# Kernel tuning notes

Measured on AMD Instinct MI355X. Metric: run time of the kernel, lower is better.

Reference implementation:

```python
import jax, jax.numpy as jnp
import numpy as np

DIM = 1024
NH = 16
HD = DIM // NH  # 64
WS = 14         # window size
DFF = 4 * DIM
EPS = 1e-6


def layernorm(x, scale, bias):
    m = jnp.mean(x, axis=-1, keepdims=True)
    v = jnp.var(x, axis=-1, keepdims=True)
    return (x - m) * jax.lax.rsqrt(v + EPS) * scale + bias


def get_rel_pos(q_size, k_size, rel_pos):
    # table size (2*WS-1, HD) matches max_rel_dist, so no resize needed
    coords = (jnp.arange(q_size)[:, None] - jnp.arange(k_size)[None, :] + (k_size - 1)).astype(jnp.int32)
    return rel_pos[coords.reshape(-1)].reshape(q_size, k_size, -1)  # (q,k,HD)


def window_partition(x):
    b, h, w, c = x.shape
    pad_h = (WS - h % WS) % WS
    pad_w = (WS - w % WS) % WS
    # faithful to source: pad_w applied on axis 1, pad_h on axis 2
    x = jnp.pad(x, ((0, 0), (0, pad_w), (0, pad_h), (0, 0)))
    hp, wp = h + pad_h, w + pad_w
    x = x.reshape(b, hp // WS, WS, wp // WS, WS, c)
    windows = x.transpose(0, 1, 3, 2, 4, 5).reshape(-1, WS, WS, c)
    return windows, (hp, wp)


def window_unpartition(windows, pad_hw, hw):
    hp, wp = pad_hw
    h, w = hw
    b = windows.shape[0] // (hp * wp // WS // WS)
    x = windows.reshape(b, hp // WS, wp // WS, WS, WS, -1)
    x = x.transpose(0, 1, 3, 2, 4, 5).reshape(b, hp, wp, -1)
    return x[:, :h, :w, :]


def attention(x, qkv_kernel, qkv_bias, rel_pos_h, rel_pos_w, proj_kernel, proj_bias):
    b, h, w, _ = x.shape
    qkv = x @ qkv_kernel + qkv_bias                                  # (b,h,w,3*DIM)
    qkv = qkv.reshape(b, h * w, 3, NH, HD).transpose(2, 0, 3, 1, 4)
    qkv = qkv.reshape(3, b * NH, h * w, HD)
    q, k, v = qkv[0], qkv[1], qkv[2]
    attn = (q * HD ** -0.5) @ k.transpose(0, 2, 1)                   # (b*NH, hw, hw)
    rh = get_rel_pos(h, h, rel_pos_h)                                # (h,h,HD)
    rw = get_rel_pos(w, w, rel_pos_w)                                # (w,w,HD)
    r_q = q.reshape(-1, h, w, HD)
    rel_h = jnp.einsum('bhwc,hkc->bhwk', r_q, rh)
    rel_w = jnp.einsum('bhwc,wkc->bhwk', r_q, rw)
    attn = (attn.reshape(-1, h, w, h, w) + rel_h[:, :, :, :, None] + rel_w[:, :, :, None, :]).reshape(-1, h * w, h * w)
    attn = jax.nn.softmax(attn, axis=-1)
    out = (attn @ v).reshape(b, NH, h, w, HD).transpose(0, 2, 3, 1, 4).reshape(b, h, w, DIM)
    return out @ proj_kernel + proj_bias


def setup_inputs() -> dict:
    key = jax.random.key(0)
    ks = jax.random.split(key, 8)
    s = 0.02
    B, H, W = 4, 64, 64
    return {
        'x': jax.random.normal(ks[0], (B, H, W, DIM), jnp.float32),
        'norm1_scale': jnp.ones((DIM,), jnp.float32),
        'norm1_bias': jnp.zeros((DIM,), jnp.float32),
        'qkv_kernel': jax.random.normal(ks[1], (DIM, 3 * DIM), jnp.float32) * s,
        'qkv_bias': jnp.zeros((3 * DIM,), jnp.float32),
        'rel_pos_h': jax.random.normal(ks[2], (2 * WS - 1, HD), jnp.float32) * s,
        'rel_pos_w': jax.random.normal(ks[3], (2 * WS - 1, HD), jnp.float32) * s,
        'proj_kernel': jax.random.normal(ks[4], (DIM, DIM), jnp.float32) * s,
        'proj_bias': jnp.zeros((DIM,), jnp.float32),
        'norm2_scale': jnp.ones((DIM,), jnp.float32),
        'norm2_bias': jnp.zeros((DIM,), jnp.float32),
        'fc1_kernel': jax.random.normal(ks[5], (DIM, DFF), jnp.float32) * s,
        'fc1_bias': jnp.zeros((DFF,), jnp.float32),
        'fc2_kernel': jax.random.normal(ks[6], (DFF, DIM), jnp.float32) * s,
        'fc2_bias': jnp.zeros((DIM,), jnp.float32),
    }


def reference(x, norm1_scale, norm1_bias, qkv_kernel, qkv_bias, rel_pos_h, rel_pos_w,
              proj_kernel, proj_bias, norm2_scale, norm2_bias,
              fc1_kernel, fc1_bias, fc2_kernel, fc2_bias):
    shortcut = x
    h, w = x.shape[1], x.shape[2]
    y = layernorm(x, norm1_scale, norm1_bias)
    y, pad_hw = window_partition(y)
    y = attention(y, qkv_kernel, qkv_bias, rel_pos_h, rel_pos_w, proj_kernel, proj_bias)
    y = window_unpartition(y, pad_hw, (h, w))
    x = shortcut + y                           # drop_path=0, no layer scale
    z = layernorm(x, norm2_scale, norm2_bias)
    z = jax.nn.gelu(z @ fc1_kernel + fc1_bias, approximate=False)
    z = z @ fc2_kernel + fc2_bias
    return x + z
```

## Files before the change

### kernel.cpp

```cpp
#include <hip/hip_runtime.h>

typedef __attribute__((ext_vector_type(8))) short bf16x8;
typedef __attribute__((ext_vector_type(4))) float f32x4;
typedef __attribute__((ext_vector_type(16))) float f32x16;

__device__ __forceinline__ float b2f(ushort u) {
    union { unsigned int i; float f; } v; v.i = ((unsigned int)u) << 16; return v.f;
}
__device__ __forceinline__ ushort f2b(float f) {
    union { float f; unsigned int i; } v; v.f = f;
    unsigned int i = v.i;
    return (ushort)((i + 0x7FFFu + ((i >> 16) & 1u)) >> 16);
}
__device__ __forceinline__ void glds16(const ushort* g, ushort* l) {
    __builtin_amdgcn_global_load_lds((const __attribute__((address_space(1))) void*)g,
                                     (__attribute__((address_space(3))) void*)l, 16, 0, 0);
}
__device__ __forceinline__ void BARX() {
    asm volatile("" ::: "memory");
    __builtin_amdgcn_s_barrier();
    asm volatile("" ::: "memory");
}

__global__ __launch_bounds__(256) void ln_kernel(const float* __restrict__ x,
                                                 const float* __restrict__ sc,
                                                 const float* __restrict__ bi,
                                                 ushort* __restrict__ y) {
    __shared__ float red[8];
    long row = blockIdx.x;
    const float* xr = x + row * 1024;
    int t = threadIdx.x;
    float4 u = *(const float4*)(xr + t * 4);
    float s = u.x + u.y + u.z + u.w;
    float q = u.x * u.x + u.y * u.y + u.z * u.z + u.w * u.w;
    for (int off = 32; off > 0; off >>= 1) {
        s += __shfl_xor(s, off);
        q += __shfl_xor(q, off);
    }
    if ((t & 63) == 0) { red[t >> 6] = s; red[4 + (t >> 6)] = q; }
    __syncthreads();
    s = red[0] + red[1] + red[2] + red[3];
    q = red[4] + red[5] + red[6] + red[7];
    float mean = s * (1.0f / 1024.0f);
    float var = q * (1.0f / 1024.0f) - mean * mean;
    float rstd = rsqrtf(fmaxf(var, 0.0f) + 1e-6f);
    int c = t * 4;
    float o0 = (u.x - mean) * rstd * sc[c + 0] + bi[c + 0];
    float o1 = (u.y - mean) * rstd * sc[c + 1] + bi[c + 1];
    float o2 = (u.z - mean) * rstd * sc[c + 2] + bi[c + 2];
    float o3 = (u.w - mean) * rstd * sc[c + 3] + bi[c + 3];
    uint2 o;
    o.x = (unsigned int)f2b(o0) | ((unsigned int)f2b(o1) << 16);
    o.y = (unsigned int)f2b(o2) | ((unsigned int)f2b(o3) << 16);
    *(uint2*)(y + row * 1024 + c) = o;
}

__global__ __launch_bounds__(256) void ln_part_kernel(const float* __restrict__ x,
                                                      const float* __restrict__ sc,
                                                      const float* __restrict__ bi,
                                                      ushort* __restrict__ wy,
                                                      int win_base, int nvalid) {
    __shared__ float red[8];
    int wt = blockIdx.x;
    int lwin = wt / 196, rr = wt % 196;
    int t = threadIdx.x;
    int valid = 0;
    long xrow = 0;
    if (lwin < nvalid) {
        int gwin = win_base + lwin;
        int img = gwin / 25, wrem = gwin % 25;
        int gh = (wrem / 5) * 14 + rr / 14;
        int gw = (wrem % 5) * 14 + rr % 14;
        if (gh < 64 && gw < 64) {
            valid = 1;
            xrow = (long)img * 4096 + gh * 64 + gw;
        }
    }
    uint2 o; o.x = 0u; o.y = 0u;
    if (valid) {
        const float* xr = x + xrow * 1024;
        float4 u = *(const float4*)(xr + t * 4);
        float s = u.x + u.y + u.z + u.w;
        float q = u.x * u.x + u.y * u.y + u.z * u.z + u.w * u.w;
        for (int off = 32; off > 0; off >>= 1) {
            s += __shfl_xor(s, off);
            q += __shfl_xor(q, off);
        }
        if ((t & 63) == 0) { red[t >> 6] = s; red[4 + (t >> 6)] = q; }
        __syncthreads();
        s = red[0] + red[1] + red[2] + red[3];
        q = red[4] + red[5] + red[6] + red[7];
        float mean = s * (1.0f / 1024.0f);
        float var = q * (1.0f / 1024.0f) - mean * mean;
        float rstd = rsqrtf(fmaxf(var, 0.0f) + 1e-6f);
        int c = t * 4;
        float o0 = (u.x - mean) * rstd * sc[c + 0] + bi[c + 0];
        float o1 = (u.y - mean) * rstd * sc[c + 1] + bi[c + 1];
        float o2 = (u.z - mean) * rstd * sc[c + 2] + bi[c + 2];
        float o3 = (u.w - mean) * rstd * sc[c + 3] + bi[c + 3];
        o.x = (unsigned int)f2b(o0) | ((unsigned int)f2b(o1) << 16);
        o.y = (unsigned int)f2b(o2) | ((unsigned int)f2b(o3) << 16);
    }
    *(uint2*)(wy + (long)wt * 1024 + t * 4) = o;
}

__global__ void transpose_w(const float* __restrict__ in, ushort* __restrict__ out,
                            int K, int N) {
    __shared__ float tile[32][33];
    int n0 = blockIdx.x * 32, k0 = blockIdx.y * 32;
    int tx = threadIdx.x, ty = threadIdx.y;
    for (int i = 0; i < 32; i += 8)
        tile[ty + i][tx] = in[(long)(k0 + ty + i) * N + n0 + tx];
    __syncthreads();
    for (int i = 0; i < 32; i += 8)
        out[(long)(n0 + ty + i) * K + k0 + tx] = f2b(tile[tx][ty + i]);
}

template <int FLAGS, typename OT>
__global__ __launch_bounds__(256) void gemm_bt(const ushort* __restrict__ A,
                                               const ushort* __restrict__ Bt,
                                               const float* __restrict__ bias,
                                               const float* __restrict__ resid,
                                               OT* __restrict__ out,
                                               int M, int N, int K) {
    __shared__ __align__(16) ushort As[128 * 32];
    __shared__ __align__(16) ushort Bs[128 * 32];
    const int tid = threadIdx.x;
    const int lane = tid & 63, w = tid >> 6;
    const int wm = (w >> 1) * 64, wn = (w & 1) * 64;
    const int quad = lane >> 4, l16 = lane & 15;
    const int bm = blockIdx.x * 128, bn = blockIdx.y * 128;
    const int r = tid >> 2, kc = (tid & 3) * 8;
    f32x4 acc[4][4];
#pragma unroll
    for (int i = 0; i < 4; i++)
#pragma unroll
        for (int j = 0; j < 4; j++) acc[i][j] = (f32x4){0.f, 0.f, 0.f, 0.f};
    const ushort* Ag = A + (long)(bm + r) * K + kc;
    const ushort* Bg = Bt + (long)(bn + r) * K + kc;
    ushort* AsW = As + w * 512;
    ushort* BsW = Bs + w * 512;
    for (int k0 = 0; k0 < K; k0 += 32) {
        __syncthreads();
        glds16(Ag + k0, AsW);
        glds16(Ag + (long)64 * K + k0, AsW + 2048);
        glds16(Bg + k0, BsW);
        glds16(Bg + (long)64 * K + k0, BsW + 2048);
        __syncthreads();
        bf16x8 afr[4], bfr[4];
#pragma unroll
        for (int t = 0; t < 4; t++) {
            afr[t] = *(const bf16x8*)&As[(wm + t * 16 + l16) * 32 + quad * 8];
            bfr[t] = *(const bf16x8*)&Bs[(wn + t * 16 + l16) * 32 + quad * 8];
        }
#pragma unroll
        for (int tm = 0; tm < 4; tm++)
#pragma unroll
            for (int tn = 0; tn < 4; tn++)
                acc[tm][tn] = __builtin_amdgcn_mfma_f32_16x16x32_bf16(afr[tm], bfr[tn],
                                                                     acc[tm][tn], 0, 0, 0);
    }
#pragma unroll
    for (int tm = 0; tm < 4; tm++) {
#pragma unroll
        for (int j = 0; j < 4; j++) {
            int gm = bm + wm + tm * 16 + quad * 4 + j;
#pragma unroll
            for (int tn = 0; tn < 4; tn++) {
                int gn = bn + wn + tn * 16 + l16;
                float v = acc[tm][tn][j] + bias[gn];
                if (FLAGS & 1) v = 0.5f * v * (1.0f + erff(v * 0.70710678118654752f));
                if (FLAGS & 2) v += resid[(long)gm * N + gn];
                if (sizeof(OT) == 4) out[(long)gm * N + gn] = (OT)v;
                else out[(long)gm * N + gn] = (OT)f2b(v);
            }
        }
    }
}

#define DSR(dst, addr, imm) \
    asm volatile("ds_read_b128 %0, %1 offset:%2" : "=&v"(dst) : "v"(addr), "n"(imm));

#define MFMA32(mf, nf, a, b) \
    acc[mf][nf] = __builtin_amdgcn_mfma_f32_32x32x16_bf16(a, b, acc[mf][nf], 0, 0, 0);

#define TILE32(bb, ts, STG, VM) do {                                                     \
    bf16x8 b00, b10, a00, a10, a20, a30, b01, b11, a01, a11, a21, a31;                   \
    DSR(b00, b_k0, (bb) * 16384 + 0)                                                     \
    DSR(b10, b_k0, (bb) * 16384 + 2048)                                                  \
    DSR(a00, a_k0, (bb) * 16384 + 0)                                                     \
    DSR(a10, a_k0, (bb) * 16384 + 2048)                                                  \
    DSR(a20, a_k0, (bb) * 16384 + 4096)                                                  \
    DSR(a30, a_k0, (bb) * 16384 + 6144)                                                  \
    DSR(b01, b_k1, (bb) * 16384 + 0)                                                     \
    DSR(b11, b_k1, (bb) * 16384 + 2048)                                                  \
    DSR(a01, a_k1, (bb) * 16384 + 0)                                                     \
    DSR(a11, a_k1, (bb) * 16384 + 2048)                                                  \
    DSR(a21, a_k1, (bb) * 16384 + 4096)                                                  \
    DSR(a31, a_k1, (bb) * 16384 + 6144)                                                  \
    if (STG) {                                                                           \
        glds16(Ag + (long)(ts) * 32, &As[((bb) + 3) & 3][sdst]);                         \
        glds16(Ag2 + (long)(ts) * 32, &As[((bb) + 3) & 3][sdst + 4096]);                 \
        glds16(Bg + (long)(ts) * 32, &Bs[((bb) + 3) & 3][sdst]);                         \
        glds16(Bg2 + (long)(ts) * 32, &Bs[((bb) + 3) & 3][sdst + 4096]);                 \
    }                                                                                    \
    __builtin_amdgcn_sched_barrier(0);                                                   \
    asm volatile("s_waitcnt lgkmcnt(6)" ::: "memory");                                   \
    __builtin_amdgcn_sched_barrier(0);                                                   \
    __builtin_amdgcn_s_setprio(1);                                                       \
    MFMA32(0, 0, a00, b00) MFMA32(0, 1, a00, b10)                                        \
    MFMA32(1, 0, a10, b00) MFMA32(1, 1, a10, b10)                                        \
    MFMA32(2, 0, a20, b00) MFMA32(2, 1, a20, b10)                                        \
    MFMA32(3, 0, a30, b00) MFMA32(3, 1, a30, b10)                                        \
    __builtin_amdgcn_s_setprio(0);                                                       \
    asm volatile("s_waitcnt lgkmcnt(0)" ::: "memory");                                   \
    __builtin_amdgcn_sched_barrier(0);                                                   \
    __builtin_amdgcn_s_setprio(1);                                                       \
    MFMA32(0, 0, a01, b01) MFMA32(0, 1, a01, b11)                                        \
    MFMA32(1, 0, a11, b01) MFMA32(1, 1, a11, b11)                                        \
    MFMA32(2, 0, a21, b01) MFMA32(2, 1, a21, b11)                                        \
    MFMA32(3, 0, a31, b01) MFMA32(3, 1, a31, b11)                                        \
    __builtin_amdgcn_s_setprio(0);                                                       \
    __builtin_amdgcn_sched_barrier(0);                                                   \
    asm volatile("s_waitcnt " VM ::: "memory");                                          \
    BARX();                                                                              \
} while (0)

template <int FLAGS, typename OT>
__global__ __launch_bounds__(512, 2) void gemm256(const ushort* __restrict__ A,
                                                  const ushort* __restrict__ Bt,
                                                  const float* __restrict__ bias,
                                                  const float* __restrict__ resid,
                                                  OT* __restrict__ out,
                                                  int M, int N, int K, int nbn) {
    __shared__ __align__(64) ushort As[4][8192];
    __shared__ __align__(64) ushort Bs[4][8192];
    const int nwg = gridDim.x;
    const int orig = blockIdx.x;
    const int q8 = nwg >> 3, r8 = nwg & 7;
    const int xcd = orig & 7, sub = orig >> 3;
    const int wgid = (xcd < r8 ? xcd * (q8 + 1) : r8 * (q8 + 1) + (xcd - r8) * q8) + sub;
    const int bm = (wgid / nbn) * 256, bn = (wgid % nbn) * 256;

    const int tid = threadIdx.x;
    const int lane = tid & 63, w = tid >> 6;
    const int l31 = lane & 31, hi = lane >> 5;
    const int wm = (w >> 2) * 128, wn = (w & 3) * 64;

    const int r_st = w * 16 + (lane >> 2);
    const int c_st = (((lane & 3) ^ ((lane >> 2) & 3) ^ ((lane >> 4) & 1)) << 3);
    const ushort* Ag = A + (long)(bm + r_st) * K + c_st;
    const ushort* Ag2 = Ag + (long)128 * K;
    const ushort* Bg = Bt + (long)(bn + r_st) * K + c_st;
    const ushort* Bg2 = Bg + (long)128 * K;
    const int sdst = w * 512;

    const int swz = (lane & 3) ^ ((lane >> 2) & 1);
    const int s0 = swz & 1, s1 = swz >> 1;
    const int slot_k0 = (((0 ^ s1) << 1) | (hi ^ s0)) << 4;
    const int slot_k1 = (((1 ^ s1) << 1) | (hi ^ s0)) << 4;
    const unsigned As0 =
        (unsigned)(size_t)(__attribute__((address_space(3))) ushort*)&As[0][0];
    const unsigned Bs0 =
        (unsigned)(size_t)(__attribute__((address_space(3))) ushort*)&Bs[0][0];
    const unsigned a_k0 = As0 + (unsigned)((wm + l31) * 64 + slot_k0);
    const unsigned a_k1 = As0 + (unsigned)((wm + l31) * 64 + slot_k1);
    const unsigned b_k0 = Bs0 + (unsigned)((wn + l31) * 64 + slot_k0);
    const unsigned b_k1 = Bs0 + (unsigned)((wn + l31) * 64 + slot_k1);

    f32x16 acc[4][2];
#pragma unroll
    for (int i = 0; i < 4; i++)
#pragma unroll
        for (int j = 0; j < 2; j++)
#pragma unroll
            for (int e = 0; e < 16; e++) acc[i][j][e] = 0.f;

    glds16(Ag, &As[0][sdst]);       glds16(Ag2, &As[0][sdst + 4096]);
    glds16(Bg, &Bs[0][sdst]);       glds16(Bg2, &Bs[0][sdst + 4096]);
    glds16(Ag + 32, &As[1][sdst]);  glds16(Ag2 + 32, &As[1][sdst + 4096]);
    glds16(Bg + 32, &Bs[1][sdst]);  glds16(Bg2 + 32, &Bs[1][sdst + 4096]);
    glds16(Ag + 64, &As[2][sdst]);  glds16(Ag2 + 64, &As[2][sdst + 4096]);
    glds16(Bg + 64, &Bs[2][sdst]);  glds16(Bg2 + 64, &Bs[2][sdst + 4096]);
    __builtin_amdgcn_sched_barrier(0);
    asm volatile("s_waitcnt vmcnt(8)" ::: "memory");
    BARX();

    const int nt = K >> 5;
    for (int t = 0; t < nt - 4; t += 4) {
        TILE32(0, t + 3, 1, "vmcnt(8)");
        TILE32(1, t + 4, 1, "vmcnt(8)");
        TILE32(2, t + 5, 1, "vmcnt(8)");
        TILE32(3, t + 6, 1, "vmcnt(8)");
    }
    TILE32(0, nt - 1, 1, "vmcnt(8)");
    TILE32(1, 0, 0, "vmcnt(4)");
    TILE32(2, 0, 0, "vmcnt(0)");
    TILE32(3, 0, 0, "vmcnt(0)");

#pragma unroll
    for (int mf = 0; mf < 4; mf++) {
#pragma unroll
        for (int nf = 0; nf < 2; nf++) {
            const int gn = bn + wn + nf * 32 + l31;
#pragma unroll
            for (int q = 0; q < 4; q++) {
#pragma unroll
                for (int j = 0; j < 4; j++) {
                    const int gm = bm + wm + mf * 32 + q * 8 + j + 4 * hi;
                    const long ro = (long)gm * N;
                    float v = acc[mf][nf][q * 4 + j] + bias[gn];
                    if (FLAGS & 1) v = 0.5f * v * (1.0f + erff(v * 0.70710678118654752f));
                    if (FLAGS & 2) v += resid[ro + gn];
                    if (sizeof(OT) == 4) out[ro + gn] = (OT)v;
                    else out[ro + gn] = (OT)f2b(v);
                }
            }
        }
    }
}

__global__ __launch_bounds__(256) void attn_kernel(const ushort* __restrict__ qkv,
                                                   ushort* __restrict__ o_out,
                                                   const float* __restrict__ relH,
                                                   const float* __restrict__ relW,
                                                   int win0, long orow0) {
    __shared__ __align__(16) ushort Vt[64 * 200];
    __shared__ __align__(16) ushort Ps[64 * 104];
    __shared__ __align__(16) ushort sc[8 * 448];
    const int head = blockIdx.y;
    const long qbase = (long)blockIdx.x * 196 * 3072 + head * 64;
    const int gwin = win0 + blockIdx.x;
    const int img = gwin / 25, wrem = gwin % 25;
    const int whh = (wrem / 5) * 14, www = (wrem % 5) * 14;
    const int tid = threadIdx.x, lane = tid & 63, w = tid >> 6;
    const int quad = lane >> 4, l16 = lane & 15;

    for (int idx = tid; idx < 196 * 64; idx += 256) {
        int k = idx >> 6, d = idx & 63;
        Vt[d * 200 + k] = qkv[qbase + 2048 + (long)k * 3072 + d];
    }
    __syncthreads();

    bf16x8 bH[2][2], bW[2][2];
#pragma unroll
    for (int nt = 0; nt < 2; nt++) {
        int n = nt * 16 + l16;
#pragma unroll
        for (int kt = 0; kt < 2; kt++) {
            bf16x8 rh = (bf16x8){0, 0, 0, 0, 0, 0, 0, 0};
            bf16x8 rw = (bf16x8){0, 0, 0, 0, 0, 0, 0, 0};
            if (n < 27) {
                const float* ph = relH + n * 64 + kt * 32 + quad * 8;
                const float* pw = relW + n * 64 + kt * 32 + quad * 8;
#pragma unroll
                for (int e = 0; e < 8; e++) {
                    rh[e] = (short)f2b(ph[e]);
                    rw[e] = (short)f2b(pw[e]);
                }
            }
            bH[nt][kt] = rh;
            bW[nt][kt] = rw;
        }
    }

    for (int tr = w; tr < 13; tr += 4) {
        int qrow = tr * 16 + l16;
        if (qrow > 195) qrow = 195;
        bf16x8 qf0 = *(const bf16x8*)(qkv + qbase + (long)qrow * 3072 + quad * 8);
        bf16x8 qf1 = *(const bf16x8*)(qkv + qbase + (long)qrow * 3072 + 32 + quad * 8);

#pragma unroll
        for (int tab = 0; tab < 2; tab++) {
#pragma unroll
            for (int nt = 0; nt < 2; nt++) {
                f32x4 a = (f32x4){0.f, 0.f, 0.f, 0.f};
                a = __builtin_amdgcn_mfma_f32_16x16x32_bf16(qf0, tab ? bW[nt][0] : bH[nt][0],
                                                            a, 0, 0, 0);
                a = __builtin_amdgcn_mfma_f32_16x16x32_bf16(qf1, tab ? bW[nt][1] : bH[nt][1],
                                                            a, 0, 0, 0);
                int col = nt * 16 + l16;
                if (col < 27) {
#pragma unroll
                    for (int j = 0; j < 4; j++)
                        sc[(w * 2 + tab) * 448 + (quad * 4 + j) * 28 + col] = f2b(a[j]);
                }
            }
        }

        f32x4 sf[13];
#pragma unroll
        for (int tc = 0; tc < 13; tc++) {
            int krow = tc * 16 + l16;
            if (krow > 195) krow = 195;
            const ushort* kp = qkv + qbase + 1024 + (long)krow * 3072 + quad * 8;
            bf16x8 kf0 = *(const bf16x8*)kp;
            bf16x8 kf1 = *(const bf16x8*)(kp + 32);
            f32x4 s = (f32x4){0.f, 0.f, 0.f, 0.f};
            s = __builtin_amdgcn_mfma_f32_16x16x32_bf16(qf0, kf0, s, 0, 0, 0);
            s = __builtin_amdgcn_mfma_f32_16x16x32_bf16(qf1, kf1, s, 0, 0, 0);
            sf[tc] = s;
        }
#pragma unroll
        for (int tc = 0; tc < 13; tc++) {
            int c = tc * 16 + l16;
            if (c < 196) {
                int kh = c / 14, kw = c - kh * 14;
#pragma unroll
                for (int j = 0; j < 4; j++) {
                    int rr = tr * 16 + quad * 4 + j;
                    if (rr > 195) rr = 195;
                    float dh = b2f(sc[(w * 2 + 0) * 448 + (quad * 4 + j) * 28 +
                                      (rr / 14 - kh + 13)]);
                    float dw = b2f(sc[(w * 2 + 1) * 448 + (quad * 4 + j) * 28 +
                                      (rr % 14 - kw + 13)]);
                    sf[tc][j] = sf[tc][j] * 0.125f + dh + dw;
                }
            } else {
#pragma unroll
                for (int j = 0; j < 4; j++) sf[tc][j] = -30000.0f;
            }
        }
        f32x4 mx = sf[0];
#pragma unroll
        for (int tc = 1; tc < 13; tc++)
#pragma unroll
            for (int j = 0; j < 4; j++) mx[j] = fmaxf(mx[j], sf[tc][j]);
        for (int off = 1; off < 16; off <<= 1)
#pragma unroll
            for (int j = 0; j < 4; j++) mx[j] = fmaxf(mx[j], __shfl_xor(mx[j], off));
        f32x4 sum = (f32x4){0.f, 0.f, 0.f, 0.f};
#pragma unroll
        for (int tc = 0; tc < 13; tc++)
#pragma unroll
            for (int j = 0; j < 4; j++) {
                float p = __expf(sf[tc][j] - mx[j]);
                sf[tc][j] = p;
                sum[j] += p;
            }
        for (int off = 1; off < 16; off <<= 1)
#pragma unroll
            for (int j = 0; j < 4; j++) sum[j] += __shfl_xor(sum[j], off);
        f32x4 linv;
#pragma unroll
        for (int j = 0; j < 4; j++) linv[j] = 1.0f / sum[j];

        f32x4 oa[4];
#pragma unroll
        for (int tn = 0; tn < 4; tn++) oa[tn] = (f32x4){0.f, 0.f, 0.f, 0.f};
#pragma unroll
        for (int tc = 0; tc < 6; tc++) {
            int c = tc * 16 + l16;
#pragma unroll
            for (int j = 0; j < 4; j++)
                Ps[(w * 16 + quad * 4 + j) * 104 + c] = f2b(sf[tc][j]);
        }
#pragma unroll
        for (int ks = 0; ks < 3; ks++) {
            bf16x8 pf = *(const bf16x8*)&Ps[(w * 16 + l16) * 104 + ks * 32 + quad * 8];
#pragma unroll
            for (int tn = 0; tn < 4; tn++) {
                bf16x8 vf = *(const bf16x8*)&Vt[(tn * 16 + l16) * 200 + ks * 32 + quad * 8];
                oa[tn] = __builtin_amdgcn_mfma_f32_16x16x32_bf16(pf, vf, oa[tn], 0, 0, 0);
            }
        }
#pragma unroll
        for (int tc = 6; tc < 13; tc++) {
            int c = tc * 16 + l16;
            if (c < 196) {
#pragma unroll
                for (int j = 0; j < 4; j++)
                    Ps[(w * 16 + quad * 4 + j) * 104 + (c - 96)] = f2b(sf[tc][j]);
            }
        }
#pragma unroll
        for (int ks = 0; ks < 3; ks++) {
            bf16x8 pf = *(const bf16x8*)&Ps[(w * 16 + l16) * 104 + ks * 32 + quad * 8];
#pragma unroll
            for (int tn = 0; tn < 4; tn++) {
                bf16x8 vf = *(const bf16x8*)&Vt[(tn * 16 + l16) * 200 + 96 + ks * 32 + quad * 8];
                oa[tn] = __builtin_amdgcn_mfma_f32_16x16x32_bf16(pf, vf, oa[tn], 0, 0, 0);
            }
        }
        for (int kk = 192; kk < 196; kk++) {
            float pj[4];
#pragma unroll
            for (int j = 0; j < 4; j++)
                pj[j] = b2f(Ps[(w * 16 + quad * 4 + j) * 104 + 96 + (kk - 192)]);
#pragma unroll
            for (int tn = 0; tn < 4; tn++) {
                float vv = b2f(Vt[(tn * 16 + l16) * 200 + kk]);
#pragma unroll
                for (int j = 0; j < 4; j++) oa[tn][j] += pj[j] * vv;
            }
        }
#pragma unroll
        for (int j = 0; j < 4; j++) {
            int rr = tr * 16 + quad * 4 + j;
            if (rr < 196) {
                int gh = whh + rr / 14, gw = www + rr % 14;
                if (gh < 64 && gw < 64) {
                    long orow = (long)img * 4096 + gh * 64 + gw - orow0;
#pragma unroll
                    for (int tn = 0; tn < 4; tn++)
                        o_out[orow * 1024 + head * 64 + tn * 16 + l16] =
                            f2b(oa[tn][j] * linv[j]);
                }
            }
        }
    }
}

extern "C" void kernel_launch(void* const* d_in, const int* in_sizes, int n_in,
                              void* d_out, int out_size, void* d_ws, size_t ws_size,
                              hipStream_t stream) {
    const float* x = (const float*)d_in[0];
    const float* n1s = (const float*)d_in[1];
    const float* n1b = (const float*)d_in[2];
    const float* qkvW = (const float*)d_in[3];
    const float* qkvB = (const float*)d_in[4];
    const float* relH = (const float*)d_in[5];
    const float* relW = (const float*)d_in[6];
    const float* projW = (const float*)d_in[7];
    const float* projB = (const float*)d_in[8];
    const float* n2s = (const float*)d_in[9];
    const float* n2b = (const float*)d_in[10];
    const float* fc1W = (const float*)d_in[11];
    const float* fc1B = (const float*)d_in[12];
    const float* fc2W = (const float*)d_in[13];
    const float* fc2B = (const float*)d_in[14];
    float* OUT = (float*)d_out;
    char* ws = (char*)d_ws;

    if (ws_size >= 221000000ULL) {
        ushort* T0  = (ushort*)(ws);
        ushort* TP  = (ushort*)(ws + 6291456ULL);
        ushort* TF1 = (ushort*)(ws + 8388608ULL);
        ushort* TF2 = (ushort*)(ws + 16777216ULL);
        ushort* W0  = (ushort*)(ws + 25165824ULL);
        ushort* QKV = (ushort*)(ws + 65536000ULL);
        ushort* AO  = (ushort*)(ws + 186646528ULL);
        ushort* Z   = (ushort*)(ws + 25165824ULL);
        ushort* H   = (ushort*)(ws + 58720256ULL);

        transpose_w<<<dim3(96, 32), dim3(32, 8), 0, stream>>>(qkvW, T0, 1024, 3072);
        transpose_w<<<dim3(32, 32), dim3(32, 8), 0, stream>>>(projW, TP, 1024, 1024);
        transpose_w<<<dim3(128, 32), dim3(32, 8), 0, stream>>>(fc1W, TF1, 1024, 4096);
        transpose_w<<<dim3(32, 128), dim3(32, 8), 0, stream>>>(fc2W, TF2, 4096, 1024);
        ln_part_kernel<<<19712, 256, 0, stream>>>(x, n1s, n1b, W0, 0, 100);
        gemm256<0, ushort><<<924, 512, 0, stream>>>(W0, T0, qkvB, nullptr, QKV,
                                                    19712, 3072, 1024, 12);
        attn_kernel<<<dim3(100, 16), 256, 0, stream>>>(QKV, AO, relH, relW, 0, 0L);
        gemm256<2, float><<<256, 512, 0, stream>>>(AO, TP, projB, x, OUT,
                                                   16384, 1024, 1024, 4);
        ln_kernel<<<16384, 256, 0, stream>>>(OUT, n2s, n2b, Z);
        gemm256<1, ushort><<<1024, 512, 0, stream>>>(Z, TF1, fc1B, nullptr, H,
                                                     16384, 4096, 1024, 16);
        gemm256<2, float><<<256, 512, 0, stream>>>(H, TF2, fc2B, OUT, OUT,
                                                   16384, 1024, 4096, 4);
    } else if (ws_size >= 100000000ULL) {
        ushort* T0  = (ushort*)(ws);
        ushort* TP  = (ushort*)(ws + 6291456ULL);
        ushort* TF1 = (ushort*)(ws + 8388608ULL);
        ushort* TF2 = (ushort*)(ws + 16777216ULL);
        ushort* AO  = (ushort*)(ws + 25165824ULL);
        ushort* W0  = (ushort*)(ws + 58720256ULL);
        ushort* QKV = (ushort*)(ws + 68943872ULL);
        ushort* Z   = (ushort*)(ws + 25165824ULL);
        ushort* H   = (ushort*)(ws + 58720256ULL);

        transpose_w<<<dim3(96, 32), dim3(32, 8), 0, stream>>>(qkvW, T0, 1024, 3072);
        transpose_w<<<dim3(32, 32), dim3(32, 8), 0, stream>>>(projW, TP, 1024, 1024);
        transpose_w<<<dim3(128, 32), dim3(32, 8), 0, stream>>>(fc1W, TF1, 1024, 4096);
        transpose_w<<<dim3(32, 128), dim3(32, 8), 0, stream>>>(fc2W, TF2, 4096, 1024);
        for (int i = 0; i < 4; i++) {
            ln_part_kernel<<<4992, 256, 0, stream>>>(x, n1s, n1b, W0, i * 25, 25);
            gemm_bt<0, ushort><<<dim3(39, 24), 256, 0, stream>>>(W0, T0, qkvB, nullptr,
                                                                 QKV, 4992, 3072, 1024);
            attn_kernel<<<dim3(25, 16), 256, 0, stream>>>(QKV, AO, relH, relW, i * 25, 0L);
        }
        gemm_bt<2, float><<<dim3(128, 8), 256, 0, stream>>>(AO, TP, projB, x, OUT,
                                                            16384, 1024, 1024);
        for (int c = 0; c < 4; c++) {
            float* xc = OUT + (long)c * 4194304;
            ln_kernel<<<4096, 256, 0, stream>>>(xc, n2s, n2b, Z);
            gemm_bt<1, ushort><<<dim3(32, 32), 256, 0, stream>>>(Z, TF1, fc1B, nullptr, H,
                                                                 4096, 4096, 1024);
            gemm_bt<2, float><<<dim3(32, 8), 256, 0, stream>>>(H, TF2, fc2B, xc, xc,
                                                               4096, 1024, 4096);
        }
    } else {
        ushort* T0 = (ushort*)(ws);
        ushort* W0 = (ushort*)(ws + 6291456ULL);
        ushort* W1 = (ushort*)(ws + 16515072ULL);
        ushort* W2 = (ushort*)(ws + 22806528ULL);
        ushort* F1 = (ushort*)(ws);
        ushort* F2 = (ushort*)(ws + 8388608ULL);
        ushort* Z  = (ushort*)(ws + 16777216ULL);
        ushort* H  = (ushort*)(ws + 18874368ULL);

        transpose_w<<<dim3(96, 32), dim3(32, 8), 0, stream>>>(qkvW, T0, 1024, 3072);
        for (int i = 0; i < 4; i++) {
            const float* xi = x + (long)i * 4194304;
            ln_part_kernel<<<4992, 256, 0, stream>>>(x, n1s, n1b, W0, i * 25, 25);
            for (int g = 0; g < 5; g++) {
                gemm_bt<0, ushort><<<dim3(8, 24), 256, 0, stream>>>(
                    W0 + (long)g * 980 * 1024, T0, qkvB, nullptr, W1, 1024, 3072, 1024);
                attn_kernel<<<dim3(5, 16), 256, 0, stream>>>(W1, W2, relH, relW,
                                                             i * 25 + g * 5, (long)i * 4096);
            }
            transpose_w<<<dim3(32, 32), dim3(32, 8), 0, stream>>>(projW, W1, 1024, 1024);
            gemm_bt<2, float><<<dim3(32, 8), 256, 0, stream>>>(
                W2, W1, projB, xi, OUT + (long)i * 4194304, 4096, 1024, 1024);
        }
        transpose_w<<<dim3(128, 32), dim3(32, 8), 0, stream>>>(fc1W, F1, 1024, 4096);
        transpose_w<<<dim3(32, 128), dim3(32, 8), 0, stream>>>(fc2W, F2, 4096, 1024);
        for (int c = 0; c < 16; c++) {
            float* xc = OUT + (long)c * 1048576;
            ln_kernel<<<1024, 256, 0, stream>>>(xc, n2s, n2b, Z);
            gemm_bt<1, ushort><<<dim3(8, 32), 256, 0, stream>>>(Z, F1, fc1B, nullptr, H,
                                                                1024, 4096, 1024);
            gemm_bt<2, float><<<dim3(8, 8), 256, 0, stream>>>(H, F2, fc2B, xc, xc,
                                                              1024, 1024, 4096);
        }
    }
}
```

Measured before the change: 901.8 us.

## Software-pipeline LDS fragment reads across k-halves and tiles in gemm256

Restructures the GEMM main loop so the LDS reads for the next k-half (including the first half of the next buffer) are issued before the MFMAs of the current half run. This overlaps ds_read latency with matrix work, and global-to-LDS staging is issued at the start of each tile. It doubles the live fragment registers, reorders the vmcnt waits, and rewrites the loop tail by hand. Register pressure and the correctness of the wait counts around the barrier are the main risks.

```diff
diff --git a/kernel.cpp b/kernel.cpp
--- a/kernel.cpp
+++ b/kernel.cpp
@@ -184,45 +184,49 @@
 #define MFMA32(mf, nf, a, b) \
     acc[mf][nf] = __builtin_amdgcn_mfma_f32_32x32x16_bf16(a, b, acc[mf][nf], 0, 0, 0);
 
-#define TILE32(bb, ts, STG, VM) do {                                                     \
-    bf16x8 b00, b10, a00, a10, a20, a30, b01, b11, a01, a11, a21, a31;                   \
-    DSR(b00, b_k0, (bb) * 16384 + 0)                                                     \
-    DSR(b10, b_k0, (bb) * 16384 + 2048)                                                  \
-    DSR(a00, a_k0, (bb) * 16384 + 0)                                                     \
-    DSR(a10, a_k0, (bb) * 16384 + 2048)                                                  \
-    DSR(a20, a_k0, (bb) * 16384 + 4096)                                                  \
-    DSR(a30, a_k0, (bb) * 16384 + 6144)                                                  \
-    DSR(b01, b_k1, (bb) * 16384 + 0)                                                     \
-    DSR(b11, b_k1, (bb) * 16384 + 2048)                                                  \
-    DSR(a01, a_k1, (bb) * 16384 + 0)                                                     \
-    DSR(a11, a_k1, (bb) * 16384 + 2048)                                                  \
-    DSR(a21, a_k1, (bb) * 16384 + 4096)                                                  \
-    DSR(a31, a_k1, (bb) * 16384 + 6144)                                                  \
-    if (STG) {                                                                           \
-        glds16(Ag + (long)(ts) * 32, &As[((bb) + 3) & 3][sdst]);                         \
-        glds16(Ag2 + (long)(ts) * 32, &As[((bb) + 3) & 3][sdst + 4096]);                 \
-        glds16(Bg + (long)(ts) * 32, &Bs[((bb) + 3) & 3][sdst]);                         \
-        glds16(Bg2 + (long)(ts) * 32, &Bs[((bb) + 3) & 3][sdst + 4096]);                 \
-    }                                                                                    \
+#define RDK0(buf) \
+    DSR(y0, b_k0, (buf) * 16384 + 0)    DSR(y1, b_k0, (buf) * 16384 + 2048) \
+    DSR(x0, a_k0, (buf) * 16384 + 0)    DSR(x1, a_k0, (buf) * 16384 + 2048) \
+    DSR(x2, a_k0, (buf) * 16384 + 4096) DSR(x3, a_k0, (buf) * 16384 + 6144)
+
+#define RDK1(buf) \
+    DSR(Y0, b_k1, (buf) * 16384 + 0)    DSR(Y1, b_k1, (buf) * 16384 + 2048) \
+    DSR(X0, a_k1, (buf) * 16384 + 0)    DSR(X1, a_k1, (buf) * 16384 + 2048) \
+    DSR(X2, a_k1, (buf) * 16384 + 4096) DSR(X3, a_k1, (buf) * 16384 + 6144)
+
+#define MFK0 \
+    MFMA32(0, 0, x0, y0) MFMA32(0, 1, x0, y1) MFMA32(1, 0, x1, y0) MFMA32(1, 1, x1, y1) \
+    MFMA32(2, 0, x2, y0) MFMA32(2, 1, x2, y1) MFMA32(3, 0, x3, y0) MFMA32(3, 1, x3, y1)
+
+#define MFK1 \
+    MFMA32(0, 0, X0, Y0) MFMA32(0, 1, X0, Y1) MFMA32(1, 0, X1, Y0) MFMA32(1, 1, X1, Y1) \
+    MFMA32(2, 0, X2, Y0) MFMA32(2, 1, X2, Y1) MFMA32(3, 0, X3, Y0) MFMA32(3, 1, X3, Y1)
+
+#define LGW6 asm volatile("s_waitcnt lgkmcnt(6)" ::: "memory"); \
+    __builtin_amdgcn_sched_barrier(0);
+
+#define STAGE4(ts, dbuf) \
+    glds16(Ag + (long)(ts) * 32, &As[dbuf][sdst]); \
+    glds16(Ag2 + (long)(ts) * 32, &As[dbuf][sdst + 4096]); \
+    glds16(Bg + (long)(ts) * 32, &Bs[dbuf][sdst]); \
+    glds16(Bg2 + (long)(ts) * 32, &Bs[dbuf][sdst + 4096]);
+
+#define TILEF(bb, ts) do {                                                               \
+    STAGE4(ts + 3, ((bb) + 3) & 3)                                                       \
     __builtin_amdgcn_sched_barrier(0);                                                   \
-    asm volatile("s_waitcnt lgkmcnt(6)" ::: "memory");                                   \
-    __builtin_amdgcn_sched_barrier(0);                                                   \
+    asm volatile("s_waitcnt vmcnt(4)" ::: "memory");                                     \
+    RDK1(bb)                                                                             \
+    LGW6                                                                                 \
     __builtin_amdgcn_s_setprio(1);                                                       \
-    MFMA32(0, 0, a00, b00) MFMA32(0, 1, a00, b10)                                        \
-    MFMA32(1, 0, a10, b00) MFMA32(1, 1, a10, b10)                                        \
-    MFMA32(2, 0, a20, b00) MFMA32(2, 1, a20, b10)                                        \
-    MFMA32(3, 0, a30, b00) MFMA32(3, 1, a30, b10)                                        \
-    __builtin_amdgcn_s_setprio(0);                                                       \
-    asm volatile("s_waitcnt lgkmcnt(0)" ::: "memory");                                   \
-    __builtin_amdgcn_sched_barrier(0);                                                   \
-    __builtin_amdgcn_s_setprio(1);                                                       \
-    MFMA32(0, 0, a01, b01) MFMA32(0, 1, a01, b11)                                        \
-    MFMA32(1, 0, a11, b01) MFMA32(1, 1, a11, b11)                                        \
-    MFMA32(2, 0, a21, b01) MFMA32(2, 1, a21, b11)                                        \
-    MFMA32(3, 0, a31, b01) MFMA32(3, 1, a31, b11)                                        \
+    MFK0                                                                                 \
     __builtin_amdgcn_s_setprio(0);                                                       \
     __builtin_amdgcn_sched_barrier(0);                                                   \
-    asm volatile("s_waitcnt " VM ::: "memory");                                          \
+    RDK0(((bb) + 1) & 3)                                                                 \
+    LGW6                                                                                 \
+    __builtin_amdgcn_s_setprio(1);                                                       \
+    MFK1                                                                                 \
+    __builtin_amdgcn_s_setprio(0);                                                       \
+    __builtin_amdgcn_sched_barrier(0);                                                   \
     BARX();                                                                              \
 } while (0)
 
@@ -276,6 +280,9 @@
 #pragma unroll
             for (int e = 0; e < 16; e++) acc[i][j][e] = 0.f;
 
+    bf16x8 x0, x1, x2, x3, y0, y1;
+    bf16x8 X0, X1, X2, X3, Y0, Y1;
+
     glds16(Ag, &As[0][sdst]);       glds16(Ag2, &As[0][sdst + 4096]);
     glds16(Bg, &Bs[0][sdst]);       glds16(Bg2, &Bs[0][sdst + 4096]);
     glds16(Ag + 32, &As[1][sdst]);  glds16(Ag2 + 32, &As[1][sdst + 4096]);
@@ -283,20 +290,44 @@
     glds16(Ag + 64, &As[2][sdst]);  glds16(Ag2 + 64, &As[2][sdst + 4096]);
     glds16(Bg + 64, &Bs[2][sdst]);  glds16(Bg2 + 64, &Bs[2][sdst + 4096]);
     __builtin_amdgcn_sched_barrier(0);
-    asm volatile("s_waitcnt vmcnt(8)" ::: "memory");
+    asm volatile("s_waitcnt vmcnt(4)" ::: "memory");
     BARX();
+    RDK0(0)
 
     const int nt = K >> 5;
-    for (int t = 0; t < nt - 4; t += 4) {
-        TILE32(0, t + 3, 1, "vmcnt(8)");
-        TILE32(1, t + 4, 1, "vmcnt(8)");
-        TILE32(2, t + 5, 1, "vmcnt(8)");
-        TILE32(3, t + 6, 1, "vmcnt(8)");
-    }
-    TILE32(0, nt - 1, 1, "vmcnt(8)");
-    TILE32(1, 0, 0, "vmcnt(4)");
-    TILE32(2, 0, 0, "vmcnt(0)");
-    TILE32(3, 0, 0, "vmcnt(0)");
+    for (int t = 0; t + 8 <= nt; t += 4) {
+        TILEF(0, t);
+        TILEF(1, t + 1);
+        TILEF(2, t + 2);
+        TILEF(3, t + 3);
+    }
+    TILEF(0, nt - 4);
+    RDK1(1)
+    LGW6
+    __builtin_amdgcn_s_setprio(1); MFK0 __builtin_amdgcn_s_setprio(0);
+    __builtin_amdgcn_sched_barrier(0);
+    RDK0(2)
+    LGW6
+    __builtin_amdgcn_s_setprio(1); MFK1 __builtin_amdgcn_s_setprio(0);
+    __builtin_amdgcn_sched_barrier(0);
+    asm volatile("s_waitcnt vmcnt(0)" ::: "memory");
+    BARX();
+    RDK1(2)
+    LGW6
+    __builtin_amdgcn_s_setprio(1); MFK0 __builtin_amdgcn_s_setprio(0);
+    __builtin_amdgcn_sched_barrier(0);
+    RDK0(3)
+    LGW6
+    __builtin_amdgcn_s_setprio(1); MFK1 __builtin_amdgcn_s_setprio(0);
+    __builtin_amdgcn_sched_barrier(0);
+    RDK1(3)
+    LGW6
+    __builtin_amdgcn_s_setprio(1); MFK0 __builtin_amdgcn_s_setprio(0);
+    __builtin_amdgcn_sched_barrier(0);
+    asm volatile("s_waitcnt lgkmcnt(0)" ::: "memory");
+    __builtin_amdgcn_sched_barrier(0);
+    __builtin_amdgcn_s_setprio(1); MFK1 __builtin_amdgcn_s_setprio(0);
+    __builtin_amdgcn_sched_barrier(0);
 
 #pragma unroll
     for (int mf = 0; mf < 4; mf++) {
```

After: 909.3 us. No clear change (+0.8%).
